# Performance work log

Measured on AMD Instinct MI355X. Metric: run time of the kernel, lower is better.

Reference implementation:

```python
import jax, jax.numpy as jnp
import numpy as np

N, M, K = 40000, 20000, 16
IN_DIM, HID, OUT_DIM, H = 64, 128, 128, 4
DH = HID // H
SIGMA_A = 15.0
FACTOR_A = 180.0 / (SIGMA_A * np.pi)  # angle (rad) -> embedding index, GeoTransformer convention
EPS = 1e-5


def sinusoidal_embed(x, d_model):
    """GeoTransformer-style sinusoidal embedding, interleaved [sin0,cos0,sin1,cos1,...]."""
    div = jnp.exp(jnp.arange(0, d_model, 2, dtype=jnp.float32) * (-np.log(10000.0) / d_model))
    omegas = x[..., None] * div  # (..., d_model/2)
    emb = jnp.stack([jnp.sin(omegas), jnp.cos(omegas)], axis=-1)
    return emb.reshape(*x.shape, d_model)


def setup_inputs() -> dict:
    key = jax.random.key(0)
    ks = jax.random.split(key, 16)

    def lin(k, i, o):
        return jax.random.normal(k, (i, o), jnp.float32) * (1.0 / np.sqrt(i))

    return {
        "feats": jax.random.normal(ks[0], (N, IN_DIM), jnp.float32),
        "node_idx": jax.random.randint(ks[1], (M,), 0, N, dtype=jnp.int32),
        "group_idx": jax.random.randint(ks[2], (M, K), 0, N, dtype=jnp.int32),
        "ppfs": jax.random.uniform(ks[3], (M, K, 4), jnp.float32, 0.0, np.pi),
        # PPF structural embedding projection
        "W_a": lin(ks[4], HID, HID), "b_a": jnp.zeros((HID,), jnp.float32),
        # input projection
        "W_in": lin(ks[5], IN_DIM, HID), "b_in": jnp.zeros((HID,), jnp.float32),
        # attention q/k/v/p projections
        "W_q": lin(ks[6], HID, HID), "b_q": jnp.zeros((HID,), jnp.float32),
        "W_k": lin(ks[7], HID, HID), "b_k": jnp.zeros((HID,), jnp.float32),
        "W_v": lin(ks[8], HID, HID), "b_v": jnp.zeros((HID,), jnp.float32),
        "W_p": lin(ks[9], HID, HID), "b_p": jnp.zeros((HID,), jnp.float32),
        # attention output linear + layernorm
        "W_o": lin(ks[10], HID, HID), "b_o": jnp.zeros((HID,), jnp.float32),
        "ln_g": jnp.ones((HID,), jnp.float32), "ln_b": jnp.zeros((HID,), jnp.float32),
        # output projection
        "W_out": lin(ks[11], HID, OUT_DIM), "b_out": jnp.zeros((OUT_DIM,), jnp.float32),
    }


def reference(feats, node_idx, group_idx, ppfs,
              W_a, b_a, W_in, b_in, W_q, b_q, W_k, b_k, W_v, b_v, W_p, b_p,
              W_o, b_o, ln_g, ln_b, W_out, b_out):
    # --- PPF structural embedding: sinusoidal per angle, linear, max over 4 angles ---
    a_emb = sinusoidal_embed(ppfs * FACTOR_A, HID)          # (M, K, 4, HID)
    a_emb = a_emb @ W_a + b_a
    pos = jnp.max(a_emb, axis=2)                            # (M, K, HID)

    # --- input projection ---
    f = feats @ W_in + b_in                                 # (N, HID)

    # --- local RPE multi-head attention ---
    q = (f @ W_q + b_q)[node_idx].reshape(M, H, DH)         # (M, H, DH)
    k = (f @ W_k + b_k)[group_idx].reshape(M, K, H, DH)     # (M, K, H, DH)
    v = (f @ W_v + b_v)[group_idx].reshape(M, K, H, DH)
    p = (pos @ W_p + b_p).reshape(M, K, H, DH)

    scores = jnp.einsum('mhd,mkhd->mhk', q, k + p) / np.sqrt(DH)  # (M, H, K)
    attn = jax.nn.softmax(scores, axis=-1)
    o = jnp.einsum('mhk,mkhd->mhd', attn, v).reshape(M, HID)

    # --- output linear + residual + layernorm ---
    hidden = o @ W_o + b_o
    res = f[node_idx] + hidden
    mu = jnp.mean(res, axis=-1, keepdims=True)
    var = jnp.var(res, axis=-1, keepdims=True)
    normed = (res - mu) * jax.lax.rsqrt(var + EPS) * ln_g + ln_b

    # --- final projection ---
    return normed @ W_out + b_out                           # (M, OUT_DIM)
```

## Files before the change

kernel.cpp:

```cpp
#include <hip/hip_runtime.h>

#define TQ 4096

__device__ __forceinline__ ushort f2bf(float x) {
  union { float f; unsigned u; } v; v.f = x;
  unsigned r = v.u + 0x7FFFu + ((v.u >> 16) & 1u);
  return (ushort)(r >> 16);
}
__device__ __forceinline__ float bflo(unsigned u) {
  union { unsigned u; float f; } v; v.u = u << 16;
  return v.f;
}
__device__ __forceinline__ float bfhi(unsigned u) {
  union { unsigned u; float f; } v; v.u = u & 0xffff0000u;
  return v.f;
}

__global__ __launch_bounds__(256) void weight_prep1(
    const float* __restrict__ W_in, const float* __restrict__ b_in,
    const float* __restrict__ W_q, const float* __restrict__ b_q,
    const float* __restrict__ W_k, const float* __restrict__ b_k,
    const float* __restrict__ W_v, const float* __restrict__ b_v,
    float* __restrict__ Wkv, float* __restrict__ bkv,
    float* __restrict__ Wbig, float* __restrict__ bbig) {
  __shared__ float WinS[64 * 128];
  __shared__ float binS[128];
  int t = threadIdx.x;
  for (int i = t; i < 8192; i += 256) WinS[i] = W_in[i];
  if (t < 128) binS[t] = b_in[t];
  __syncthreads();
  const float* W; const float* b;
  int which = blockIdx.x;
  if (which == 0) { W = W_q; b = b_q; }
  else if (which == 1) { W = W_k; b = b_k; }
  else { W = W_v; b = b_v; }
  int c = t & 127, ih = t >> 7;
  float acc[32] = {};
  float bacc = 0.f;
  for (int o = 0; o < 128; ++o) {
    float wv = W[o * 128 + c];
    bacc += binS[o] * wv;
#pragma unroll
    for (int j = 0; j < 32; ++j) acc[j] += WinS[(ih * 32 + j) * 128 + o] * wv;
  }
  bacc += b[c];
  if (which == 0) {
#pragma unroll
    for (int j = 0; j < 32; ++j) {
      int i = ih * 32 + j;
      Wbig[i * 768 + c] = acc[j];
      Wbig[i * 768 + 128 + c] = WinS[i * 128 + c];
    }
    if (ih == 0) { bbig[c] = bacc; bbig[128 + c] = binS[c]; }
  } else if (which == 1) {
#pragma unroll
    for (int j = 0; j < 32; ++j) Wkv[(ih * 32 + j) * 256 + c] = acc[j];
    if (ih == 0) bkv[c] = bacc;
  } else {
#pragma unroll
    for (int j = 0; j < 32; ++j) Wkv[(ih * 32 + j) * 256 + 128 + c] = acc[j];
    if (ih == 0) bkv[128 + c] = bacc;
  }
}

__global__ __launch_bounds__(256) void weight_prep2(
    const float* __restrict__ W_p, float* Wbig, float* bbig) {
  __shared__ float WcqS[64][33];
  __shared__ float bcqS[32];
  int t = threadIdx.x;
  int blk = blockIdx.x;
  int h = blk >> 1;
  for (int idx = t; idx < 2048; idx += 256) {
    int i = idx >> 5, d = idx & 31;
    WcqS[i][d] = Wbig[i * 768 + h * 32 + d];
  }
  if (t < 32) bcqS[t] = bbig[h * 32 + t];
  __syncthreads();
  int hc = blk * 64 + (t & 63);
  int c = hc & 127;
  int rg = t >> 6;
  float acc[16] = {};
  float bacc = 0.f;
  for (int d = 0; d < 32; ++d) {
    float wp = W_p[c * 128 + h * 32 + d];
    bacc += bcqS[d] * wp;
#pragma unroll
    for (int j = 0; j < 16; ++j) acc[j] += WcqS[rg * 16 + j][d] * wp;
  }
#pragma unroll
  for (int j = 0; j < 16; ++j) Wbig[(rg * 16 + j) * 768 + 256 + hc] = acc[j];
  if (rg == 0) bbig[256 + hc] = bacc;
}

__global__ __launch_bounds__(256) void mega_proj(
    const float* __restrict__ feats, const int* __restrict__ node_idx,
    const float* __restrict__ Wkv, const float* __restrict__ bkv,
    const float* __restrict__ Wbig, const float* __restrict__ bbig,
    const float* __restrict__ W_a, const float* __restrict__ b_a,
    ushort* __restrict__ kvb, float* __restrict__ mrow,
    ushort* __restrict__ qpb, float* __restrict__ T) {
  __shared__ float smem[64 * 20];
  int t = threadIdx.x;
  int b = blockIdx.x;
  if (b < 2500) {
    float (*fTS)[20] = (float(*)[20])smem;
    int row0 = b * 16;
#pragma unroll
    for (int ii = 0; ii < 4; ++ii) {
      int idx = ii * 256 + t;
      int r = idx >> 6, i = idx & 63;
      fTS[i][r] = feats[(size_t)(row0 + r) * 64 + i];
    }
    __syncthreads();
    int c = t;
    float bv = bkv[c];
    float acc[16];
#pragma unroll
    for (int j = 0; j < 16; ++j) acc[j] = bv;
    for (int i = 0; i < 64; ++i) {
      float w = Wkv[i * 256 + c];
      float fv[16];
      *(float4*)&fv[0]  = *(const float4*)&fTS[i][0];
      *(float4*)&fv[4]  = *(const float4*)&fTS[i][4];
      *(float4*)&fv[8]  = *(const float4*)&fTS[i][8];
      *(float4*)&fv[12] = *(const float4*)&fTS[i][12];
#pragma unroll
      for (int j = 0; j < 16; ++j) acc[j] += fv[j] * w;
    }
#pragma unroll
    for (int j = 0; j < 16; ++j)
      kvb[(size_t)(row0 + j) * 256 + c] = f2bf(acc[j]);
  } else if (b < 5000) {
    float (*fTS)[12] = (float(*)[12])smem;
    int m0 = (b - 2500) * 8;
#pragma unroll
    for (int ii = 0; ii < 2; ++ii) {
      int idx = ii * 256 + t;
      int r = idx >> 6, i = idx & 63;
      int ni = node_idx[m0 + r];
      fTS[i][r] = feats[(size_t)ni * 64 + i];
    }
    __syncthreads();
    int c = t;
    float a0[8], a1[8], a2[8];
    float b0 = bbig[c], b1 = bbig[256 + c], b2 = bbig[512 + c];
#pragma unroll
    for (int j = 0; j < 8; ++j) { a0[j] = b0; a1[j] = b1; a2[j] = b2; }
    for (int i = 0; i < 64; ++i) {
      float w0 = Wbig[i * 768 + c];
      float w1 = Wbig[i * 768 + 256 + c];
      float w2 = Wbig[i * 768 + 512 + c];
      float fv[8];
      *(float4*)&fv[0] = *(const float4*)&fTS[i][0];
      *(float4*)&fv[4] = *(const float4*)&fTS[i][4];
#pragma unroll
      for (int j = 0; j < 8; ++j) {
        a0[j] += fv[j] * w0; a1[j] += fv[j] * w1; a2[j] += fv[j] * w2;
      }
    }
#pragma unroll
    for (int j = 0; j < 8; ++j) {
      int m = m0 + j;
      mrow[(size_t)m * 256 + c] = a0[j];
      qpb[(size_t)m * 512 + c] = f2bf(a1[j]);
      qpb[(size_t)m * 512 + 256 + c] = f2bf(a2[j]);
    }
  } else {
    float (*sS)[64] = (float(*)[64])smem;
    float (*cS)[64] = (float(*)[64])(smem + 512);
    int row0 = (b - 5000) * 8;
    for (int i = t; i < 512; i += 256) {
      int r = i >> 6, j = i & 63;
      float x = (float)(row0 + r) * (12.0f / (float)(TQ - 1));
      float theta = expf(-(float)j * (9.210340371976184f / 64.0f));
      float om = x * theta;
      sS[r][j] = sinf(om);
      cS[r][j] = cosf(om);
    }
    __syncthreads();
    int c = t & 127, half = t >> 7;
    float bb = b_a[c];
    float a0 = bb, a1 = bb, a2 = bb, a3 = bb;
    int r = half * 4;
    for (int j = 0; j < 64; ++j) {
      float ws = W_a[(2 * j) * 128 + c];
      float wc = W_a[(2 * j + 1) * 128 + c];
      a0 += sS[r + 0][j] * ws + cS[r + 0][j] * wc;
      a1 += sS[r + 1][j] * ws + cS[r + 1][j] * wc;
      a2 += sS[r + 2][j] * ws + cS[r + 2][j] * wc;
      a3 += sS[r + 3][j] * ws + cS[r + 3][j] * wc;
    }
    int rr = row0 + r;
    T[(size_t)(rr + 0) * 128 + c] = a0;
    T[(size_t)(rr + 1) * 128 + c] = a1;
    T[(size_t)(rr + 2) * 128 + c] = a2;
    T[(size_t)(rr + 3) * 128 + c] = a3;
  }
}

__global__ __launch_bounds__(256) void attn_fused(
    const ushort* __restrict__ kvb, const float* __restrict__ mrow,
    const ushort* __restrict__ qpb, const float* __restrict__ T,
    const float* __restrict__ ppfs, const int* __restrict__ group_idx,
    float* __restrict__ o_out) {
  __shared__ unsigned posW[4][16][68];
  __shared__ unsigned qpW[4][4][68];
  __shared__ float qW[4][4][36];
  __shared__ float attnW[4][64];
  __shared__ float ppfW[4][64];
  __shared__ int gW[4][16];

  int t = threadIdx.x;
  int w = t >> 6;
  int lane = t & 63;
  int m = blockIdx.x * 4 + w;

  ppfW[w][lane] = ppfs[(size_t)m * 64 + lane];
  if (lane < 16) gW[w][lane] = group_idx[m * 16 + lane];
  const float* mr = mrow + (size_t)m * 256;
  {
    float q0 = mr[lane];
    float q1 = mr[64 + lane];
    qW[w][lane >> 5][lane & 31] = q0;
    int c1 = 64 + lane;
    qW[w][c1 >> 5][c1 & 31] = q1;
  }
  {
    uint4 qpu = ((const uint4*)(qpb + (size_t)m * 512))[lane];
    int j = lane * 4;
    int h = j >> 6, j2 = j & 63;
    qpW[w][h][j2 + 0] = qpu.x;
    qpW[w][h][j2 + 1] = qpu.y;
    qpW[w][h][j2 + 2] = qpu.z;
    qpW[w][h][j2 + 3] = qpu.w;
  }
  __syncthreads();

  const float TS = (float)(TQ - 1) / 12.0f;
  int c0 = lane * 2;
#pragma unroll 4
  for (int k = 0; k < 16; ++k) {
    float p0 = -1e30f, p1 = -1e30f;
#pragma unroll
    for (int a = 0; a < 4; ++a) {
      float x = ppfW[w][k * 4 + a] * 3.8197186342054885f;
      float u = x * TS;
      int i0 = (int)u;
      i0 = min(i0, TQ - 2);
      float fr = u - (float)i0;
      const float* Tp = T + (size_t)i0 * 128 + c0;
      float2 t0 = *(const float2*)Tp;
      float2 t1 = *(const float2*)(Tp + 128);
      p0 = fmaxf(p0, t0.x + fr * (t1.x - t0.x));
      p1 = fmaxf(p1, t0.y + fr * (t1.y - t0.y));
    }
    posW[w][k][lane] = (unsigned)f2bf(p0) | ((unsigned)f2bf(p1) << 16);
  }
  __syncthreads();

  {
    int h = lane >> 4, k = lane & 15;
    int g = gW[w][k];
    const uint4* kp = (const uint4*)(kvb + (size_t)g * 256 + h * 32);
    float s = 0.f;
#pragma unroll
    for (int d8 = 0; d8 < 4; ++d8) {
      uint4 kk = kp[d8];
      float4 qv0 = *(const float4*)&qW[w][h][d8 * 8];
      float4 qv1 = *(const float4*)&qW[w][h][d8 * 8 + 4];
      s += qv0.x * bflo(kk.x) + qv0.y * bfhi(kk.x) +
           qv0.z * bflo(kk.y) + qv0.w * bfhi(kk.y) +
           qv1.x * bflo(kk.z) + qv1.y * bfhi(kk.z) +
           qv1.z * bflo(kk.w) + qv1.w * bfhi(kk.w);
    }
#pragma unroll 8
    for (int c4 = 0; c4 < 32; ++c4) {
      unsigned pu0 = posW[w][k][2 * c4], pu1 = posW[w][k][2 * c4 + 1];
      unsigned qu0 = qpW[w][h][2 * c4], qu1 = qpW[w][h][2 * c4 + 1];
      s += bflo(pu0) * bflo(qu0) + bfhi(pu0) * bfhi(qu0) +
           bflo(pu1) * bflo(qu1) + bfhi(pu1) * bfhi(qu1);
    }
    s *= 0.17677669529663687f;
    float mx = s;
#pragma unroll
    for (int off = 1; off < 16; off <<= 1) mx = fmaxf(mx, __shfl_xor(mx, off));
    float e = __expf(s - mx);
    float sum = e;
#pragma unroll
    for (int off = 1; off < 16; off <<= 1) sum += __shfl_xor(sum, off);
    attnW[w][lane] = e / sum;
  }
  __syncthreads();

  {
    float o0 = 0.f, o1 = 0.f;
    int h0 = lane >> 4;
#pragma unroll
    for (int k = 0; k < 16; ++k) {
      float aw = attnW[w][h0 * 16 + k];
      unsigned vv = *(const unsigned*)(kvb + (size_t)gW[w][k] * 256 + 128 + c0);
      o0 += aw * bflo(vv);
      o1 += aw * bfhi(vv);
    }
    *(float2*)&o_out[(size_t)m * 128 + c0] = make_float2(o0, o1);
  }
}

__global__ __launch_bounds__(256) void final_fused(
    const float* __restrict__ o, const float* __restrict__ mrow,
    const float* __restrict__ W_o, const float* __restrict__ b_o,
    const float* __restrict__ ln_g, const float* __restrict__ ln_b,
    const float* __restrict__ W_out, const float* __restrict__ b_out,
    float* __restrict__ out) {
  __shared__ float oS[16 * 128];
  __shared__ float rS[16 * 128];
  __shared__ float redS[16][2][2];
  int t = threadIdx.x;
  int m0 = blockIdx.x * 16;
  for (int i = t; i < 2048; i += 256) oS[i] = o[(size_t)m0 * 128 + i];
  __syncthreads();
  int c = t & 127, half = t >> 7;
  float acc[8];
  {
    float bv = b_o[c];
#pragma unroll
    for (int j = 0; j < 8; ++j) acc[j] = bv;
  }
  for (int i = 0; i < 128; ++i) {
    float wv = W_o[i * 128 + c];
#pragma unroll
    for (int j = 0; j < 8; ++j) acc[j] += oS[(half * 8 + j) * 128 + i] * wv;
  }
#pragma unroll
  for (int j = 0; j < 8; ++j)
    acc[j] += mrow[(size_t)(m0 + half * 8 + j) * 256 + 128 + c];
  int wih = (t >> 6) & 1;
#pragma unroll
  for (int j = 0; j < 8; ++j) {
    float s1 = acc[j], s2 = acc[j] * acc[j];
#pragma unroll
    for (int off = 1; off < 64; off <<= 1) {
      s1 += __shfl_xor(s1, off);
      s2 += __shfl_xor(s2, off);
    }
    if ((t & 63) == 0) {
      redS[half * 8 + j][wih][0] = s1;
      redS[half * 8 + j][wih][1] = s2;
    }
  }
  __syncthreads();
  float gv = ln_g[c], lb = ln_b[c];
#pragma unroll
  for (int j = 0; j < 8; ++j) {
    int row = half * 8 + j;
    float s1 = redS[row][0][0] + redS[row][1][0];
    float s2 = redS[row][0][1] + redS[row][1][1];
    float mean = s1 * (1.0f / 128.0f);
    float var = s2 * (1.0f / 128.0f) - mean * mean;
    float rstd = rsqrtf(var + 1e-5f);
    rS[row * 128 + c] = (acc[j] - mean) * rstd * gv + lb;
  }
  __syncthreads();
  float acc2[8];
  {
    float b2 = b_out[c];
#pragma unroll
    for (int j = 0; j < 8; ++j) acc2[j] = b2;
  }
  for (int i = 0; i < 128; ++i) {
    float wv = W_out[i * 128 + c];
#pragma unroll
    for (int j = 0; j < 8; ++j) acc2[j] += rS[(half * 8 + j) * 128 + i] * wv;
  }
#pragma unroll
  for (int j = 0; j < 8; ++j)
    out[(size_t)(m0 + half * 8 + j) * 128 + c] = acc2[j];
}

extern "C" void kernel_launch(void* const* d_in, const int* in_sizes, int n_in,
                              void* d_out, int out_size, void* d_ws, size_t ws_size,
                              hipStream_t stream) {
  const float* feats    = (const float*)d_in[0];
  const int*   node_idx = (const int*)d_in[1];
  const int*   group_idx= (const int*)d_in[2];
  const float* ppfs     = (const float*)d_in[3];
  const float* W_a      = (const float*)d_in[4];
  const float* b_a      = (const float*)d_in[5];
  const float* W_in     = (const float*)d_in[6];
  const float* b_in     = (const float*)d_in[7];
  const float* W_q      = (const float*)d_in[8];
  const float* b_q      = (const float*)d_in[9];
  const float* W_k      = (const float*)d_in[10];
  const float* b_k      = (const float*)d_in[11];
  const float* W_v      = (const float*)d_in[12];
  const float* b_v      = (const float*)d_in[13];
  const float* W_p      = (const float*)d_in[14];
  const float* W_o      = (const float*)d_in[16];
  const float* b_o      = (const float*)d_in[17];
  const float* ln_g     = (const float*)d_in[18];
  const float* ln_b     = (const float*)d_in[19];
  const float* W_out    = (const float*)d_in[20];
  const float* b_out    = (const float*)d_in[21];
  float* out = (float*)d_out;

  float* ws   = (float*)d_ws;
  ushort* kvb = (ushort*)ws;
  float* mrow = ws + 5120000;
  ushort* qpb = (ushort*)(ws + 10240000);
  float* T    = ws + 15360000;
  float* o    = ws + 15884288;
  float* Wkv  = ws + 18444288;
  float* bkv  = ws + 18460672;
  float* Wbig = ws + 18460928;
  float* bbig = ws + 18510080;

  weight_prep1<<<3, 256, 0, stream>>>(W_in, b_in, W_q, b_q, W_k, b_k, W_v, b_v,
                                      Wkv, bkv, Wbig, bbig);
  weight_prep2<<<8, 256, 0, stream>>>(W_p, Wbig, bbig);
  mega_proj<<<5512, 256, 0, stream>>>(feats, node_idx, Wkv, bkv, Wbig, bbig,
                                      W_a, b_a, kvb, mrow, qpb, T);
  attn_fused<<<20000 / 4, 256, 0, stream>>>(kvb, mrow, qpb, T, ppfs, group_idx, o);
  final_fused<<<20000 / 16, 256, 0, stream>>>(o, mrow, W_o, b_o, ln_g, ln_b,
                                              W_out, b_out, out);
}
```

Measured before the change: 331.6 us.

## Interleave adjacent PPF table rows and drop block barriers in attention kernel

The angle-embedding table is rebuilt so each float4 holds two channels for both row i and row i+1. Each interpolation tap then needs one 16-byte gather instead of two separate 8-byte loads. In the attention kernel the block-wide barriers are removed, relying on each wavefront touching only its own shared-memory slice. The positional-embedding buffer is halved by computing it in two batches of eight neighbours, interleaved with the score dot products, which lowers LDS use. The trade-offs are a table twice as large and reliance on implicit lockstep execution within a wavefront for correctness.

```diff
diff --git a/kernel.cpp b/kernel.cpp
--- a/kernel.cpp
+++ b/kernel.cpp
@@ -98,7 +98,7 @@
     const float* __restrict__ Wbig, const float* __restrict__ bbig,
     const float* __restrict__ W_a, const float* __restrict__ b_a,
     ushort* __restrict__ kvb, float* __restrict__ mrow,
-    ushort* __restrict__ qpb, float* __restrict__ T) {
+    ushort* __restrict__ qpb, float4* __restrict__ Tq) {
   __shared__ float smem[64 * 20];
   int t = threadIdx.x;
   int b = blockIdx.x;
@@ -167,9 +167,9 @@
     }
   } else {
     float (*sS)[64] = (float(*)[64])smem;
-    float (*cS)[64] = (float(*)[64])(smem + 512);
+    float (*cS)[64] = (float(*)[64])(smem + 576);
     int row0 = (b - 5000) * 8;
-    for (int i = t; i < 512; i += 256) {
+    for (int i = t; i < 576; i += 256) {
       int r = i >> 6, j = i & 63;
       float x = (float)(row0 + r) * (12.0f / (float)(TQ - 1));
       float theta = expf(-(float)j * (9.210340371976184f / 64.0f));
@@ -178,32 +178,42 @@
       cS[r][j] = cosf(om);
     }
     __syncthreads();
-    int c = t & 127, half = t >> 7;
-    float bb = b_a[c];
-    float a0 = bb, a1 = bb, a2 = bb, a3 = bb;
-    int r = half * 4;
+    int cp = t & 63;
+    int qr = t >> 6;
+    int c0 = cp * 2, c1 = c0 + 1;
+    float g0[3], g1[3];
+    {
+      float bb0 = b_a[c0], bb1 = b_a[c1];
+#pragma unroll
+      for (int r = 0; r < 3; ++r) { g0[r] = bb0; g1[r] = bb1; }
+    }
     for (int j = 0; j < 64; ++j) {
-      float ws = W_a[(2 * j) * 128 + c];
-      float wc = W_a[(2 * j + 1) * 128 + c];
-      a0 += sS[r + 0][j] * ws + cS[r + 0][j] * wc;
-      a1 += sS[r + 1][j] * ws + cS[r + 1][j] * wc;
-      a2 += sS[r + 2][j] * ws + cS[r + 2][j] * wc;
-      a3 += sS[r + 3][j] * ws + cS[r + 3][j] * wc;
-    }
-    int rr = row0 + r;
-    T[(size_t)(rr + 0) * 128 + c] = a0;
-    T[(size_t)(rr + 1) * 128 + c] = a1;
-    T[(size_t)(rr + 2) * 128 + c] = a2;
-    T[(size_t)(rr + 3) * 128 + c] = a3;
+      float ws0 = W_a[(2 * j) * 128 + c0];
+      float wc0 = W_a[(2 * j + 1) * 128 + c0];
+      float ws1 = W_a[(2 * j) * 128 + c1];
+      float wc1 = W_a[(2 * j + 1) * 128 + c1];
+#pragma unroll
+      for (int r = 0; r < 3; ++r) {
+        int rr = qr * 2 + r;
+        float sv = sS[rr][j], cv = cS[rr][j];
+        g0[r] += sv * ws0 + cv * wc0;
+        g1[r] += sv * ws1 + cv * wc1;
+      }
+    }
+#pragma unroll
+    for (int r = 0; r < 2; ++r) {
+      int row = row0 + qr * 2 + r;
+      Tq[(size_t)row * 64 + cp] = make_float4(g0[r], g1[r], g0[r + 1], g1[r + 1]);
+    }
   }
 }
 
 __global__ __launch_bounds__(256) void attn_fused(
     const ushort* __restrict__ kvb, const float* __restrict__ mrow,
-    const ushort* __restrict__ qpb, const float* __restrict__ T,
+    const ushort* __restrict__ qpb, const float4* __restrict__ Tq,
     const float* __restrict__ ppfs, const int* __restrict__ group_idx,
     float* __restrict__ o_out) {
-  __shared__ unsigned posW[4][16][68];
+  __shared__ unsigned posW[4][8][68];
   __shared__ unsigned qpW[4][4][68];
   __shared__ float qW[4][4][36];
   __shared__ float attnW[4][64];
@@ -228,41 +238,19 @@
   {
     uint4 qpu = ((const uint4*)(qpb + (size_t)m * 512))[lane];
     int j = lane * 4;
-    int h = j >> 6, j2 = j & 63;
-    qpW[w][h][j2 + 0] = qpu.x;
-    qpW[w][h][j2 + 1] = qpu.y;
-    qpW[w][h][j2 + 2] = qpu.z;
-    qpW[w][h][j2 + 3] = qpu.w;
-  }
-  __syncthreads();
-
-  const float TS = (float)(TQ - 1) / 12.0f;
-  int c0 = lane * 2;
-#pragma unroll 4
-  for (int k = 0; k < 16; ++k) {
-    float p0 = -1e30f, p1 = -1e30f;
-#pragma unroll
-    for (int a = 0; a < 4; ++a) {
-      float x = ppfW[w][k * 4 + a] * 3.8197186342054885f;
-      float u = x * TS;
-      int i0 = (int)u;
-      i0 = min(i0, TQ - 2);
-      float fr = u - (float)i0;
-      const float* Tp = T + (size_t)i0 * 128 + c0;
-      float2 t0 = *(const float2*)Tp;
-      float2 t1 = *(const float2*)(Tp + 128);
-      p0 = fmaxf(p0, t0.x + fr * (t1.x - t0.x));
-      p1 = fmaxf(p1, t0.y + fr * (t1.y - t0.y));
-    }
-    posW[w][k][lane] = (unsigned)f2bf(p0) | ((unsigned)f2bf(p1) << 16);
-  }
-  __syncthreads();
-
-  {
-    int h = lane >> 4, k = lane & 15;
-    int g = gW[w][k];
+    int hh = j >> 6, j2 = j & 63;
+    qpW[w][hh][j2 + 0] = qpu.x;
+    qpW[w][hh][j2 + 1] = qpu.y;
+    qpW[w][hh][j2 + 2] = qpu.z;
+    qpW[w][hh][j2 + 3] = qpu.w;
+  }
+
+  int h = lane >> 4, k = lane & 15;
+  int g = gW[w][k];
+
+  float s = 0.f;
+  {
     const uint4* kp = (const uint4*)(kvb + (size_t)g * 256 + h * 32);
-    float s = 0.f;
 #pragma unroll
     for (int d8 = 0; d8 < 4; ++d8) {
       uint4 kk = kp[d8];
@@ -273,13 +261,39 @@
            qv1.x * bflo(kk.z) + qv1.y * bfhi(kk.z) +
            qv1.z * bflo(kk.w) + qv1.w * bfhi(kk.w);
     }
+  }
+
+  const float TS = (float)(TQ - 1) / 12.0f;
+  for (int kb = 0; kb < 2; ++kb) {
+#pragma unroll
+    for (int k2 = 0; k2 < 8; ++k2) {
+      int kk = kb * 8 + k2;
+      float p0 = -1e30f, p1 = -1e30f;
+#pragma unroll
+      for (int a = 0; a < 4; ++a) {
+        float x = ppfW[w][kk * 4 + a] * 3.8197186342054885f;
+        float u = x * TS;
+        int i0 = min((int)u, TQ - 2);
+        float fr = u - (float)i0;
+        float4 tv = Tq[(size_t)i0 * 64 + lane];
+        p0 = fmaxf(p0, tv.x + fr * (tv.z - tv.x));
+        p1 = fmaxf(p1, tv.y + fr * (tv.w - tv.y));
+      }
+      posW[w][k2][lane] = (unsigned)f2bf(p0) | ((unsigned)f2bf(p1) << 16);
+    }
+    if ((k >> 3) == kb) {
+      int k2 = k & 7;
 #pragma unroll 8
-    for (int c4 = 0; c4 < 32; ++c4) {
-      unsigned pu0 = posW[w][k][2 * c4], pu1 = posW[w][k][2 * c4 + 1];
-      unsigned qu0 = qpW[w][h][2 * c4], qu1 = qpW[w][h][2 * c4 + 1];
-      s += bflo(pu0) * bflo(qu0) + bfhi(pu0) * bfhi(qu0) +
-           bflo(pu1) * bflo(qu1) + bfhi(pu1) * bfhi(qu1);
-    }
+      for (int c4 = 0; c4 < 32; ++c4) {
+        unsigned pu0 = posW[w][k2][2 * c4], pu1 = posW[w][k2][2 * c4 + 1];
+        unsigned qu0 = qpW[w][h][2 * c4], qu1 = qpW[w][h][2 * c4 + 1];
+        s += bflo(pu0) * bflo(qu0) + bfhi(pu0) * bfhi(qu0) +
+             bflo(pu1) * bflo(qu1) + bfhi(pu1) * bfhi(qu1);
+      }
+    }
+  }
+
+  {
     s *= 0.17677669529663687f;
     float mx = s;
 #pragma unroll
@@ -290,15 +304,15 @@
     for (int off = 1; off < 16; off <<= 1) sum += __shfl_xor(sum, off);
     attnW[w][lane] = e / sum;
   }
-  __syncthreads();
-
-  {
+
+  {
+    int c0 = lane * 2;
     float o0 = 0.f, o1 = 0.f;
     int h0 = lane >> 4;
 #pragma unroll
-    for (int k = 0; k < 16; ++k) {
-      float aw = attnW[w][h0 * 16 + k];
-      unsigned vv = *(const unsigned*)(kvb + (size_t)gW[w][k] * 256 + 128 + c0);
+    for (int kk = 0; kk < 16; ++kk) {
+      float aw = attnW[w][h0 * 16 + kk];
+      unsigned vv = *(const unsigned*)(kvb + (size_t)gW[w][kk] * 256 + 128 + c0);
       o0 += aw * bflo(vv);
       o1 += aw * bfhi(vv);
     }
@@ -407,19 +421,19 @@
   ushort* kvb = (ushort*)ws;
   float* mrow = ws + 5120000;
   ushort* qpb = (ushort*)(ws + 10240000);
-  float* T    = ws + 15360000;
-  float* o    = ws + 15884288;
-  float* Wkv  = ws + 18444288;
-  float* bkv  = ws + 18460672;
-  float* Wbig = ws + 18460928;
-  float* bbig = ws + 18510080;
+  float4* Tq  = (float4*)(ws + 15360000);
+  float* o    = ws + 16408576;
+  float* Wkv  = ws + 18968576;
+  float* bkv  = ws + 18984960;
+  float* Wbig = ws + 18985216;
+  float* bbig = ws + 19034368;
 
   weight_prep1<<<3, 256, 0, stream>>>(W_in, b_in, W_q, b_q, W_k, b_k, W_v, b_v,
                                       Wkv, bkv, Wbig, bbig);
   weight_prep2<<<8, 256, 0, stream>>>(W_p, Wbig, bbig);
   mega_proj<<<5512, 256, 0, stream>>>(feats, node_idx, Wkv, bkv, Wbig, bbig,
-                                      W_a, b_a, kvb, mrow, qpb, T);
-  attn_fused<<<20000 / 4, 256, 0, stream>>>(kvb, mrow, qpb, T, ppfs, group_idx, o);
+                                      W_a, b_a, kvb, mrow, qpb, Tq);
+  attn_fused<<<20000 / 4, 256, 0, stream>>>(kvb, mrow, qpb, Tq, ppfs, group_idx, o);
   final_fused<<<20000 / 16, 256, 0, stream>>>(o, mrow, W_o, b_o, ln_g, ln_b,
                                               W_out, b_out, out);
 }
```

Result: faster. 309.8 us (-6.6%).
